# Optimization experiments

Measured on AMD Instinct MI355X. Metric: run time of the kernel, lower is better.

The kernel has to match this reference:

```python
import jax, jax.numpy as jnp
import numpy as np

N_PIX = 596   # (151-2)*(6-2) after two VALID 2x2 convs
HEADS, D = 4, 64

def _ln(x, axes, g=None, b=None, eps=1e-5):
    mu = jnp.mean(x, axes, keepdims=True)
    var = jnp.var(x, axes, keepdims=True)
    y = (x - mu) * jax.lax.rsqrt(var + eps)
    return y * g + b if g is not None else y

def _conv(x, w, b):
    y = jax.lax.conv_general_dilated(x, w, (1, 1), 'VALID',
                                     dimension_numbers=('NCHW', 'OIHW', 'NCHW'))
    return y + b[None, :, None, None]


def setup_inputs() -> dict:
    key = jax.random.key(0)
    ks = jax.random.split(key, 24)
    f32 = jnp.float32
    w = lambda k, s: jax.random.normal(k, s, f32) * 0.05
    inp = {
        'x': jax.random.normal(ks[0], (64, 4, 151, 6), f32),
        'conv1_w': w(ks[1], (16, 4, 2, 2)),  'conv1_b': w(ks[2], (16,)),
        'conv2_w': w(ks[3], (32, 16, 2, 2)), 'conv2_b': w(ks[4], (32,)),
        'kp_w': w(ks[5], (34, 256)),  'kp_b': w(ks[6], (256,)),
        'qp_w': w(ks[7], (34, 256)),  'qp_b': w(ks[8], (256,)),
        'vp_w': w(ks[9], (34, 256)),  'vp_b': w(ks[10], (256,)),
        'klin_w': w(ks[11], (64, N_PIX)), 'klin_b': w(ks[12], (N_PIX,)),
        'qlin_w': w(ks[13], (64, N_PIX)), 'qlin_b': w(ks[14], (N_PIX,)),
        'alin_w': w(ks[15], (N_PIX, N_PIX)), 'alin_b': w(ks[16], (N_PIX,)),
        'knorm_g': jnp.ones((HEADS, N_PIX, D), f32), 'knorm_b': jnp.zeros((HEADS, N_PIX, D), f32),
        'qnorm_g': jnp.ones((HEADS, N_PIX, D), f32), 'qnorm_b': jnp.zeros((HEADS, N_PIX, D), f32),
        'vnorm_g': jnp.ones((HEADS, N_PIX, D), f32), 'vnorm_b': jnp.zeros((HEADS, N_PIX, D), f32),
        'lin1_w': w(ks[17], (256, 64)), 'lin1_b': w(ks[18], (64,)),
        'lin2_w': w(ks[19], (64, 10)),  'lin2_b': w(ks[20], (10,)),
    }
    return inp


def reference(x, conv1_w, conv1_b, conv2_w, conv2_b,
              kp_w, kp_b, qp_w, qp_b, vp_w, vp_b,
              klin_w, klin_b, qlin_w, qlin_b, alin_w, alin_b,
              knorm_g, knorm_b, qnorm_g, qnorm_b, vnorm_g, vnorm_b,
              lin1_w, lin1_b, lin2_w, lin2_b):
    h = jax.nn.relu(_conv(x, conv1_w, conv1_b))
    h = jax.nn.relu(_conv(h, conv2_w, conv2_b))          # (N,32,149,4)
    N, C, cH, cW = h.shape
    xc = jnp.broadcast_to(jnp.arange(cW, dtype=h.dtype) / cW, (cH, cW))
    yc = jnp.broadcast_to((jnp.arange(cH, dtype=h.dtype) / cH)[:, None], (cH, cW))
    sp = jnp.broadcast_to(jnp.stack([xc, yc])[None], (N, 2, cH, cW))
    feats = jnp.concatenate([h, sp], axis=1).transpose(0, 2, 3, 1).reshape(N, N_PIX, C + 2)
    proj = lambda w_, b_: (feats @ w_ + b_).reshape(N, N_PIX, HEADS, D).transpose(0, 2, 1, 3)
    K = _ln(proj(kp_w, kp_b), (1, 2, 3), knorm_g, knorm_b)   # (N,h,596,64)
    Q = _ln(proj(qp_w, qp_b), (1, 2, 3), qnorm_g, qnorm_b)
    V = _ln(proj(vp_w, vp_b), (1, 2, 3), vnorm_g, vnorm_b)
    A = jax.nn.elu((Q @ qlin_w + qlin_b) + (K @ klin_w + klin_b))  # (N,h,596,596)
    A = jax.nn.softmax(A @ alin_w + alin_b, axis=-1)
    E = jnp.einsum('bhfc,bhcd->bhfd', A, V)                  # (N,h,596,64)
    E = E.transpose(0, 2, 1, 3).reshape(N, N_PIX, HEADS * D)
    E = jax.nn.relu(E @ lin1_w + lin1_b)
    E = _ln(E, (1, 2))                                       # LN over [596,64], no affine
    E = jnp.max(E, axis=1)                                   # (N,64)
    return jax.nn.elu(E @ lin2_w + lin2_b)                   # (N,10)
```

## Files before the change

kernel.cpp:

```cpp
#include <hip/hip_runtime.h>
#include <hip/hip_bf16.h>
#include <math.h>

typedef __hip_bfloat16 bf16;
typedef unsigned short ushort;
typedef __attribute__((ext_vector_type(8))) short short8;
typedef __attribute__((ext_vector_type(4))) float float4v;

#define BATCH 64
#define NPIX 596
#define CH 34
#define PC 256

static __device__ __forceinline__ ushort f2bu(float v){ bf16 h = __float2bfloat16(v); return *(ushort*)&h; }
static __device__ __forceinline__ float bu2f(ushort u){ bf16 h = *(bf16*)&u; return __bfloat162float(h); }
static __device__ __forceinline__ float eluf(float x){ return x > 0.f ? x : expm1f(x); }

__global__ __launch_bounds__(256) void k_conv_feats(
    const float* __restrict__ x,
    const float* __restrict__ w1, const float* __restrict__ b1,
    const float* __restrict__ w2, const float* __restrict__ b2,
    ushort* __restrict__ featsH, ushort* __restrict__ featsL)
{
  __shared__ float sw1[256];
  __shared__ float sb1[16];
  __shared__ float sw2[2048];
  __shared__ float sb2[32];
  __shared__ float h1[16*20*5];
  const int s = blockIdx.x, b = blockIdx.y, t = threadIdx.x;
  const float* xb = x + (size_t)b * 4*151*6;

  const int p0 = s*75;
  const int p1 = (p0+75 < NPIX) ? p0+75 : NPIX;
  const int rA = p0>>2, rB = (p1-1)>>2;
  const int nh = rB - rA + 2;

  sw1[t]=w1[t];
  if (t<16) sb1[t]=b1[t];
  for (int i=t;i<2048;i+=256) sw2[i]=w2[i];
  if (t<32) sb2[t]=b2[t];
  __syncthreads();

  for (int i=t; i<16*nh*5; i+=256){
    int oc = i/(nh*5), rem = i - oc*(nh*5);
    int lr = rem/5, cc = rem - (rem/5)*5;
    int r = rA + lr;
    float acc = sb1[oc];
    #pragma unroll
    for (int ic=0;ic<4;ic++){
      const float* xp = xb + ic*906 + r*6 + cc;
      const float* wp = sw1 + oc*16 + ic*4;
      acc += xp[0]*wp[0] + xp[1]*wp[1] + xp[6]*wp[2] + xp[7]*wp[3];
    }
    h1[(oc*20 + lr)*5 + cc] = fmaxf(acc, 0.f);
  }
  __syncthreads();

  const int np = p1 - p0;
  ushort* fbH = featsH + (size_t)b*NPIX*64;
  ushort* fbL = featsL + (size_t)b*NPIX*64;
  const short8 z8 = {0,0,0,0,0,0,0,0};
  for (int i=t;i<np*4;i+=256){
    int pl = i>>2, off = 32 + (i&3)*8;
    int p = p0 + pl;
    *(short8*)(fbH + (size_t)p*64 + off) = z8;
    *(short8*)(fbL + (size_t)p*64 + off) = z8;
  }
  for (int i=t;i<32*np;i+=256){
    int oc = i/np, pl = i - oc*np;
    int p = p0 + pl;
    int r = p>>2, cc = p&3;
    int lr = r - rA;
    float acc = sb2[oc];
    #pragma unroll
    for (int ic=0;ic<16;ic++){
      const float* hp = h1 + (ic*20 + lr)*5 + cc;
      const float* wp = sw2 + oc*64 + ic*4;
      acc += hp[0]*wp[0] + hp[1]*wp[1] + hp[5]*wp[2] + hp[6]*wp[3];
    }
    float v = fmaxf(acc, 0.f);
    ushort hu = f2bu(v);
    fbH[(size_t)p*64+oc] = hu;
    fbL[(size_t)p*64+oc] = f2bu(v - bu2f(hu));
  }
  __syncthreads();
  for (int pl=t; pl<np; pl+=256){
    int p = p0 + pl;
    float v1 = (float)(p&3)*0.25f;
    float v2 = (float)(p>>2)*(1.0f/149.0f);
    ushort h1u = f2bu(v1), h2u = f2bu(v2);
    fbH[(size_t)p*64+32] = h1u;  fbL[(size_t)p*64+32] = f2bu(v1 - bu2f(h1u));
    fbH[(size_t)p*64+33] = h2u;  fbL[(size_t)p*64+33] = f2bu(v2 - bu2f(h2u));
  }
}

__global__ __launch_bounds__(256) void k_prep(
    const float* __restrict__ aw, const float* __restrict__ qw, const float* __restrict__ kw,
    const float* __restrict__ l1w,
    const float* __restrict__ kpw, const float* __restrict__ qpw, const float* __restrict__ vpw,
    ushort* __restrict__ alinP, ushort* __restrict__ WqkP, ushort* __restrict__ w1T,
    ushort* __restrict__ projP)
{
  __shared__ float sA[4][32][17];
  const int t = threadIdx.x, w = t>>6, l = t&63;
  const int gw = blockIdx.x*4 + w;

  if (gw < 1016){
    const float* src; ushort* dst;
    int row0, col0, nrow, ncol, rstride; size_t slot;
    if (gw < 760){
      int tile = gw/19, kk = gw - tile*19;
      src = aw; rstride = NPIX; nrow = NPIX; ncol = NPIX;
      row0 = kk*32; col0 = tile*16;
      dst = alinP; slot = (size_t)gw*64;
    } else if (gw < 920){
      int g1 = gw - 760;
      int tile = g1>>2, kk = g1&3;
      rstride = NPIX; nrow = 64; ncol = NPIX;
      col0 = tile*16;
      if (kk < 2){ src = qw; row0 = kk*32; }
      else       { src = kw; row0 = (kk-2)*32; }
      dst = WqkP; slot = (size_t)g1*64;
    } else {
      int g2 = gw - 920;
      int which = g2>>5, rem = g2&31;
      int tile = rem>>1, kk = rem&1;
      src = which==0 ? kpw : which==1 ? qpw : vpw;
      rstride = PC; nrow = CH; ncol = PC;
      row0 = kk*32; col0 = tile*16;
      dst = projP; slot = (size_t)g2*64;
    }
    #pragma unroll
    for (int p=0;p<2;p++){
      int rr = p*16 + (l>>2);
      int r = row0 + rr;
      int cb = (l&3)*4;
      #pragma unroll
      for (int j=0;j<4;j++){
        int c = col0 + cb + j;
        float v = (r < nrow && c < ncol) ? src[(size_t)r*rstride + c] : 0.f;
        sA[w][rr][cb + j] = v;
      }
    }
    __syncthreads();
    int nloc = l&15, c0 = (l>>4)*8;
    ushort out[8];
    #pragma unroll
    for (int i=0;i<8;i++) out[i] = f2bu(sA[w][c0+i][nloc]);
    *(short8*)(dst + (slot + l)*8) = *(short8*)out;
  } else {
    int s3 = (gw - 1016)*64 + l;
    int n = s3>>5, e0 = (s3&31)*8;
    ushort out[8];
    #pragma unroll
    for (int i=0;i<8;i++) out[i] = f2bu(l1w[(size_t)(e0+i)*64 + n]);
    *(short8*)(w1T + (size_t)s3*8) = *(short8*)out;
  }
}

__global__ __launch_bounds__(256) void k_proj_p1(
    const ushort* __restrict__ featsH, const ushort* __restrict__ featsL,
    const ushort* __restrict__ projP,
    const float* __restrict__ kpb, const float* __restrict__ qpb, const float* __restrict__ vpb,
    float* __restrict__ statsP)
{
  __shared__ float red[8];
  const int rb = blockIdx.x, b = blockIdx.y, which = blockIdx.z;
  const int t = threadIdx.x, w = t>>6, l = t&63, quad = l>>4, ln = l&15;
  const float* Bv = which==0 ? kpb : which==1 ? qpb : vpb;

  float4v acc[4][4];
  #pragma unroll
  for (int ms=0;ms<4;ms++)
    #pragma unroll
    for (int i=0;i<4;i++) acc[ms][i] = (float4v){0.f,0.f,0.f,0.f};

  #pragma unroll
  for (int kk=0;kk<4;kk++){
    const ushort* fb = (kk<2 ? featsH : featsL) + (size_t)b*NPIX*64;
    short8 aq[4];
    #pragma unroll
    for (int ms=0;ms<4;ms++){
      int r = rb*64 + ms*16 + ln;
      short8 z = {0,0,0,0,0,0,0,0};
      aq[ms] = (r < NPIX) ? *(const short8*)(fb + (size_t)r*64 + (kk&1)*32 + quad*8) : z;
    }
    #pragma unroll
    for (int i=0;i<4;i++){
      int tile = w + 4*i;
      short8 bf = *(const short8*)(projP + ((size_t)((which*16 + tile)*2 + (kk&1))*64 + l)*8);
      #pragma unroll
      for (int ms=0;ms<4;ms++)
        acc[ms][i] = __builtin_amdgcn_mfma_f32_16x16x32_bf16(aq[ms], bf, acc[ms][i], 0,0,0);
    }
  }
  float s=0.f, s2=0.f;
  #pragma unroll
  for (int i=0;i<4;i++){
    int col = (w+4*i)*16 + ln;
    float bc = Bv[col];
    #pragma unroll
    for (int ms=0;ms<4;ms++)
      #pragma unroll
      for (int r=0;r<4;r++){
        int p = rb*64 + ms*16 + quad*4 + r;
        if (p < NPIX){
          float v = acc[ms][i][r] + bc;
          s += v; s2 += v*v;
        }
      }
  }
  #pragma unroll
  for (int o=32;o>0;o>>=1){ s += __shfl_down(s,o); s2 += __shfl_down(s2,o); }
  if (l==0){ red[w]=s; red[4+w]=s2; }
  __syncthreads();
  if (t==0){
    atomicAdd(&statsP[(which*64+b)*2],   red[0]+red[1]+red[2]+red[3]);
    atomicAdd(&statsP[(which*64+b)*2+1], red[4]+red[5]+red[6]+red[7]);
  }
}

__global__ __launch_bounds__(256) void k_proj_p2(
    const ushort* __restrict__ featsH, const ushort* __restrict__ featsL,
    const ushort* __restrict__ projP,
    const float* __restrict__ kpb, const float* __restrict__ qpb, const float* __restrict__ vpb,
    const float* __restrict__ kg, const float* __restrict__ kb_,
    const float* __restrict__ qg, const float* __restrict__ qb_,
    const float* __restrict__ vg, const float* __restrict__ vb_,
    const float* __restrict__ statsP,
    ushort* __restrict__ Kb, ushort* __restrict__ Qb, ushort* __restrict__ VP)
{
  __shared__ ushort vtile[64*264];
  const int rb = blockIdx.x, b = blockIdx.y, which = blockIdx.z;
  const int t = threadIdx.x, w = t>>6, l = t&63, quad = l>>4, ln = l&15;
  const float* Bv = which==0 ? kpb : which==1 ? qpb : vpb;
  const float* G  = which==0 ? kg  : which==1 ? qg  : vg;
  const float* Be = which==0 ? kb_ : which==1 ? qb_ : vb_;

  float4v acc[4][4];
  #pragma unroll
  for (int ms=0;ms<4;ms++)
    #pragma unroll
    for (int i=0;i<4;i++) acc[ms][i] = (float4v){0.f,0.f,0.f,0.f};

  #pragma unroll
  for (int kk=0;kk<4;kk++){
    const ushort* fb = (kk<2 ? featsH : featsL) + (size_t)b*NPIX*64;
    short8 aq[4];
    #pragma unroll
    for (int ms=0;ms<4;ms++){
      int r = rb*64 + ms*16 + ln;
      short8 z = {0,0,0,0,0,0,0,0};
      aq[ms] = (r < NPIX) ? *(const short8*)(fb + (size_t)r*64 + (kk&1)*32 + quad*8) : z;
    }
    #pragma unroll
    for (int i=0;i<4;i++){
      int tile = w + 4*i;
      short8 bf = *(const short8*)(projP + ((size_t)((which*16 + tile)*2 + (kk&1))*64 + l)*8);
      #pragma unroll
      for (int ms=0;ms<4;ms++)
        acc[ms][i] = __builtin_amdgcn_mfma_f32_16x16x32_bf16(aq[ms], bf, acc[ms][i], 0,0,0);
    }
  }
  const float n = (float)(NPIX*PC);
  const float S  = statsP[(which*64+b)*2];
  const float S2 = statsP[(which*64+b)*2+1];
  const float mu = S/n;
  const float rs = rsqrtf(S2/n - mu*mu + 1e-5f);

  if (which < 2){
    ushort* out = which==0 ? Kb : Qb;
    #pragma unroll
    for (int i=0;i<4;i++){
      int col = (w+4*i)*16 + ln;
      int h = col>>6, d = col&63;
      float bc = Bv[col];
      #pragma unroll
      for (int ms=0;ms<4;ms++)
        #pragma unroll
        for (int r=0;r<4;r++){
          int p = rb*64 + ms*16 + quad*4 + r;
          if (p < NPIX){
            int gi = (h*NPIX+p)*64 + d;
            float y = (acc[ms][i][r] + bc - mu)*rs*G[gi] + Be[gi];
            out[((size_t)(b*4+h)*NPIX + p)*64 + d] = f2bu(y);
          }
        }
    }
  } else {
    #pragma unroll
    for (int i=0;i<4;i++){
      int col = (w+4*i)*16 + ln;
      int h = col>>6, d = col&63;
      float bc = Bv[col];
      #pragma unroll
      for (int ms=0;ms<4;ms++)
        #pragma unroll
        for (int r=0;r<4;r++){
          int lrow = ms*16 + quad*4 + r;
          int p = rb*64 + lrow;
          ushort o = 0;
          if (p < NPIX){
            int gi = (h*NPIX+p)*64 + d;
            o = f2bu((acc[ms][i][r] + bc - mu)*rs*G[gi] + Be[gi]);
          }
          vtile[lrow*264 + col] = o;
        }
    }
    __syncthreads();
    #pragma unroll
    for (int e=0;e<8;e++){
      int sid = e*256 + t;
      int l2 = sid & 63;
      int rest = sid >> 6;
      int kkL = rest & 1, w2 = (rest>>1)&3, hh = rest>>3;
      int kk = rb*2 + kkL;
      if (kk < 19){
        int lrow0 = kkL*32 + ((l2>>4)<<3);
        int col = hh*64 + w2*16 + (l2&15);
        ushort o[8];
        #pragma unroll
        for (int jj=0;jj<8;jj++) o[jj] = vtile[(lrow0+jj)*264 + col];
        *(short8*)(VP + ((size_t)(b*4+hh)*4864 + (w2*19 + kk)*64 + l2)*8) = *(short8*)o;
      }
    }
  }
}

__global__ __launch_bounds__(256, 2) void k_attn(
    const ushort* __restrict__ Qb, const ushort* __restrict__ Kb,
    const ushort* __restrict__ alinP, const ushort* __restrict__ WqkP,
    const ushort* __restrict__ VP,
    const float* __restrict__ qbias, const float* __restrict__ kbias,
    const float* __restrict__ abias,
    ushort* __restrict__ Ew)
{
  extern __shared__ __align__(16) ushort sm[];
  ushort* strip = sm;
  float*  red   = (float*)(sm + 39424);

  const int t = threadIdx.x;
  const int w = t>>6, l = t&63, quad = l>>4, ln = l&15;
  const int id  = blockIdx.x + blockIdx.y*10;
  const int xcd = id & 7, idx = id >> 3;
  const int lin = xcd*320 + idx;
  const int bh  = lin/10, rb = lin - bh*10;
  const int b = bh>>2, h = bh&3;
  const int row0 = rb*64;
  const ushort* Qp = Qb + (size_t)bh*NPIX*64;
  const ushort* Kp = Kb + (size_t)bh*NPIX*64;

  float4v acc[4][10];
  #pragma unroll
  for (int ms=0;ms<4;ms++)
    #pragma unroll
    for (int i=0;i<10;i++) acc[ms][i] = (float4v){0.f,0.f,0.f,0.f};

  #pragma unroll
  for (int kk=0;kk<4;kk++){
    short8 aq[4];
    #pragma unroll
    for (int ms=0;ms<4;ms++){
      int r = row0 + ms*16 + ln;
      short8 z = {0,0,0,0,0,0,0,0};
      aq[ms] = (r < NPIX)
        ? *(const short8*)((kk<2 ? Qp : Kp) + (size_t)r*64 + (kk&1)*32 + quad*8) : z;
    }
    __builtin_amdgcn_s_setprio(1);
    #pragma unroll
    for (int i=0;i<10;i++){
      int tile = w + 4*i;
      short8 bf = *(const short8*)(WqkP + ((size_t)(tile*4 + kk)*64 + l)*8);
      #pragma unroll
      for (int ms=0;ms<4;ms++)
        acc[ms][i] = __builtin_amdgcn_mfma_f32_16x16x32_bf16(aq[ms], bf, acc[ms][i], 0,0,0);
    }
    __builtin_amdgcn_s_setprio(0);
  }
  #pragma unroll
  for (int i=0;i<10;i++){
    int t0 = w + 4*i;
    if (t0 < 38){
      int col = t0*16 + ln;
      bool cv = col < NPIX;
      float qkb = cv ? (qbias[col] + kbias[col]) : 0.f;
      #pragma unroll
      for (int ms=0;ms<4;ms++)
        #pragma unroll
        for (int r=0;r<4;r++){
          float v = 0.f;
          if (cv){ float xx = acc[ms][i][r] + qkb; v = xx > 0.f ? xx : __expf(xx) - 1.f; }
          strip[(ms*16+quad*4+r)*616 + col] = f2bu(v);
        }
    }
  }
  __syncthreads();

  #pragma unroll
  for (int ms=0;ms<4;ms++)
    #pragma unroll
    for (int i=0;i<10;i++) acc[ms][i] = (float4v){0.f,0.f,0.f,0.f};
  #pragma unroll 4
  for (int kk=0;kk<19;kk++){
    short8 af[4];
    #pragma unroll
    for (int ms=0;ms<4;ms++)
      af[ms] = *(const short8*)(strip + (ms*16+ln)*616 + kk*32 + quad*8);
    __builtin_amdgcn_s_setprio(1);
    #pragma unroll
    for (int i=0;i<10;i++){
      int tile = w + 4*i;
      short8 bf = *(const short8*)(alinP + ((size_t)(tile*19 + kk)*64 + l)*8);
      #pragma unroll
      for (int ms=0;ms<4;ms++)
        acc[ms][i] = __builtin_amdgcn_mfma_f32_16x16x32_bf16(af[ms], bf, acc[ms][i], 0,0,0);
    }
    __builtin_amdgcn_s_setprio(0);
  }
  __syncthreads();

  float sum[4][4];
  #pragma unroll
  for (int ms=0;ms<4;ms++)
    #pragma unroll
    for (int r=0;r<4;r++) sum[ms][r] = 0.f;
  #pragma unroll
  for (int i=0;i<10;i++){
    int t0 = w + 4*i;
    if (t0 < 38){
      int col = t0*16 + ln;
      bool cv = col < NPIX;
      float ab = cv ? abias[col] : 0.f;
      #pragma unroll
      for (int ms=0;ms<4;ms++)
        #pragma unroll
        for (int r=0;r<4;r++){
          float e = cv ? __expf(acc[ms][i][r] + ab) : 0.f;
          sum[ms][r] += e;
          strip[(ms*16+quad*4+r)*616 + col] = f2bu(e);
        }
    }
  }
  #pragma unroll
  for (int ms=0;ms<4;ms++)
    #pragma unroll
    for (int r=0;r<4;r++)
      #pragma unroll
      for (int o=8;o>0;o>>=1) sum[ms][r] += __shfl_xor(sum[ms][r], o, 16);
  if (ln==0){
    #pragma unroll
    for (int ms=0;ms<4;ms++)
      #pragma unroll
      for (int r=0;r<4;r++) red[(ms*16+quad*4+r)*4 + w] = sum[ms][r];
  }
  __syncthreads();

  float4v ve[4];
  #pragma unroll
  for (int ms=0;ms<4;ms++) ve[ms] = (float4v){0.f,0.f,0.f,0.f};
  #pragma unroll
  for (int kk=0;kk<19;kk++){
    short8 bf = *(const short8*)(VP + ((size_t)bh*4864 + (w*19 + kk)*64 + l)*8);
    __builtin_amdgcn_s_setprio(1);
    #pragma unroll
    for (int ms=0;ms<4;ms++){
      short8 af = *(const short8*)(strip + (ms*16+ln)*616 + kk*32 + quad*8);
      ve[ms] = __builtin_amdgcn_mfma_f32_16x16x32_bf16(af, bf, ve[ms], 0,0,0);
    }
    __builtin_amdgcn_s_setprio(0);
  }
  #pragma unroll
  for (int ms=0;ms<4;ms++)
    #pragma unroll
    for (int r=0;r<4;r++){
      int p = row0 + ms*16 + quad*4 + r;
      if (p < NPIX){
        float4v v = *(float4v*)&red[(ms*16+quad*4+r)*4];
        float inv = 1.f / (v[0]+v[1]+v[2]+v[3]);
        Ew[((size_t)b*NPIX + p)*256 + h*64 + w*16 + ln] = f2bu(ve[ms][r] * inv);
      }
    }
}

__global__ __launch_bounds__(256) void k_lin1(
    const ushort* __restrict__ Ew, const ushort* __restrict__ w1T,
    const float* __restrict__ bias,
    float* __restrict__ F, float* __restrict__ stats)
{
  __shared__ ushort sw1[64*264];
  __shared__ float red[8];
  const int t = threadIdx.x;
  const int w = t>>6, l = t&63, quad = l>>4, ln = l&15;
  const int rb = blockIdx.x, b = blockIdx.y;
  for (int g=t; g<2048; g+=256){
    int row = g>>5, q = g&31;
    *(short8*)(sw1 + row*264 + q*8) = *(const short8*)(w1T + row*256 + q*8);
  }
  __syncthreads();
  float4v acc[4];
  #pragma unroll
  for (int ms=0;ms<4;ms++) acc[ms] = (float4v){0.f,0.f,0.f,0.f};
  #pragma unroll
  for (int kk=0;kk<8;kk++){
    short8 bf = *(const short8*)(sw1 + (w*16+ln)*264 + kk*32 + quad*8);
    #pragma unroll
    for (int ms=0;ms<4;ms++){
      int p = rb*64 + ms*16 + ln;
      size_t rowi = (size_t)b*NPIX + (p < NPIX ? p : 0);
      short8 a = *(const short8*)(Ew + rowi*256 + kk*32 + quad*8);
      acc[ms] = __builtin_amdgcn_mfma_f32_16x16x32_bf16(a, bf, acc[ms], 0,0,0);
    }
  }
  const int col = w*16 + ln;
  const float bc = bias[col];
  float s=0.f, s2=0.f;
  #pragma unroll
  for (int ms=0;ms<4;ms++)
    #pragma unroll
    for (int r=0;r<4;r++){
      int p = rb*64 + ms*16 + quad*4 + r;
      if (p < NPIX){
        float v = fmaxf(acc[ms][r] + bc, 0.f);
        F[((size_t)b*NPIX + p)*64 + col] = v;
        s += v; s2 += v*v;
      }
    }
  #pragma unroll
  for (int o=32;o>0;o>>=1){ s += __shfl_down(s,o); s2 += __shfl_down(s2,o); }
  if (l==0){ red[w]=s; red[4+w]=s2; }
  __syncthreads();
  if (t==0){
    atomicAdd(&stats[b*2],   red[0]+red[1]+red[2]+red[3]);
    atomicAdd(&stats[b*2+1], red[4]+red[5]+red[6]+red[7]);
  }
}

__global__ __launch_bounds__(256) void k_final(
    const float* __restrict__ F, const float* __restrict__ stats,
    const float* __restrict__ w2, const float* __restrict__ b2v,
    float* __restrict__ out)
{
  __shared__ float cm[256];
  __shared__ float nm[64];
  const int b = blockIdx.x, t = threadIdx.x;
  const int d = t&63, grp = t>>6;
  const float* Fb = F + (size_t)b*NPIX*64;
  float m = -1e30f;
  for (int p=grp;p<NPIX;p+=4) m = fmaxf(m, Fb[p*64+d]);
  cm[t]=m;
  __syncthreads();
  if (t<64){
    float mm = fmaxf(fmaxf(cm[t],cm[t+64]), fmaxf(cm[t+128],cm[t+192]));
    const float n = (float)(NPIX*64);
    float S = stats[b*2], S2 = stats[b*2+1];
    float mu = S/n, var = S2/n - mu*mu;
    nm[t] = (mm - mu) * rsqrtf(var + 1e-5f);
  }
  __syncthreads();
  if (t<10){
    float acc = b2v[t];
    for (int e=0;e<64;e++) acc += nm[e]*w2[e*10+t];
    out[b*10+t] = eluf(acc);
  }
}

extern "C" void kernel_launch(void* const* d_in, const int* in_sizes, int n_in,
                              void* d_out, int out_size, void* d_ws, size_t ws_size,
                              hipStream_t stream)
{
  const float* x       = (const float*)d_in[0];
  const float* conv1_w = (const float*)d_in[1];
  const float* conv1_b = (const float*)d_in[2];
  const float* conv2_w = (const float*)d_in[3];
  const float* conv2_b = (const float*)d_in[4];
  const float* kp_w    = (const float*)d_in[5];
  const float* kp_b    = (const float*)d_in[6];
  const float* qp_w    = (const float*)d_in[7];
  const float* qp_b    = (const float*)d_in[8];
  const float* vp_w    = (const float*)d_in[9];
  const float* vp_b    = (const float*)d_in[10];
  const float* klin_w  = (const float*)d_in[11];
  const float* klin_b  = (const float*)d_in[12];
  const float* qlin_w  = (const float*)d_in[13];
  const float* qlin_b  = (const float*)d_in[14];
  const float* alin_w  = (const float*)d_in[15];
  const float* alin_b  = (const float*)d_in[16];
  const float* knorm_g = (const float*)d_in[17];
  const float* knorm_b = (const float*)d_in[18];
  const float* qnorm_g = (const float*)d_in[19];
  const float* qnorm_b = (const float*)d_in[20];
  const float* vnorm_g = (const float*)d_in[21];
  const float* vnorm_b = (const float*)d_in[22];
  const float* lin1_w  = (const float*)d_in[23];
  const float* lin1_b  = (const float*)d_in[24];
  const float* lin2_w  = (const float*)d_in[25];
  const float* lin2_b  = (const float*)d_in[26];

  float* feats  = (float*)d_ws;
  float* F      = feats + (size_t)BATCH*NPIX*CH;
  float* statsE = F + (size_t)BATCH*NPIX*64;
  float* statsP = statsE + 128;
  ushort* Qb    = (ushort*)(statsP + 384);
  ushort* Kb    = Qb + (size_t)BATCH*4*NPIX*64;
  ushort* Vb    = Kb + (size_t)BATCH*4*NPIX*64;
  ushort* Ew    = Vb + (size_t)BATCH*4*NPIX*64;
  ushort* w1T   = Ew + (size_t)BATCH*NPIX*256;
  ushort* alinP = w1T + 16384;
  ushort* WqkP  = alinP + 389120;
  ushort* VP    = WqkP + 81920;
  ushort* projP = VP + 9961472;
  ushort* featsH = (ushort*)feats;
  ushort* featsL = (ushort*)F;

  hipMemsetAsync(statsE, 0, 512*sizeof(float), stream);

  dim3 gc(8, BATCH);
  k_conv_feats<<<gc, 256, 0, stream>>>(x, conv1_w, conv1_b, conv2_w, conv2_b, featsH, featsL);

  k_prep<<<262, 256, 0, stream>>>(alin_w, qlin_w, klin_w, lin1_w, kp_w, qp_w, vp_w,
                                  alinP, WqkP, w1T, projP);

  dim3 gp(10, BATCH, 3);
  k_proj_p1<<<gp, 256, 0, stream>>>(featsH, featsL, projP, kp_b, qp_b, vp_b, statsP);
  k_proj_p2<<<gp, 256, 0, stream>>>(featsH, featsL, projP, kp_b, qp_b, vp_b,
                                    knorm_g, knorm_b, qnorm_g, qnorm_b, vnorm_g, vnorm_b,
                                    statsP, Kb, Qb, VP);

  static bool attr_set = false;
  if (!attr_set){
    hipFuncSetAttribute((const void*)k_attn, hipFuncAttributeMaxDynamicSharedMemorySize, 79872);
    attr_set = true;
  }

  dim3 ga(10, BATCH*4);
  k_attn<<<ga, 256, 79872, stream>>>(Qb, Kb, alinP, WqkP, VP,
                                     qlin_b, klin_b, alin_b, Ew);

  dim3 gl(10, BATCH);
  k_lin1<<<gl, 256, 0, stream>>>(Ew, w1T, lin1_b, F, statsE);

  k_final<<<BATCH, 256, 0, stream>>>(F, statsE, lin2_w, lin2_b, (float*)d_out);
}
```

Before: 601.9 us.

## Split attention block across eight waves and divide PV reduction across halves

```diff
diff --git a/kernel.cpp b/kernel.cpp
--- a/kernel.cpp
+++ b/kernel.cpp
@@ -327,7 +327,7 @@
   }
 }
 
-__global__ __launch_bounds__(256, 2) void k_attn(
+__global__ __launch_bounds__(512, 4) void k_attn(
     const ushort* __restrict__ Qb, const ushort* __restrict__ Kb,
     const ushort* __restrict__ alinP, const ushort* __restrict__ WqkP,
     const ushort* __restrict__ VP,
@@ -338,6 +338,7 @@
   extern __shared__ __align__(16) ushort sm[];
   ushort* strip = sm;
   float*  red   = (float*)(sm + 39424);
+  float*  rsum  = (float*)(sm + 40448);
 
   const int t = threadIdx.x;
   const int w = t>>6, l = t&63, quad = l>>4, ln = l&15;
@@ -350,11 +351,11 @@
   const ushort* Qp = Qb + (size_t)bh*NPIX*64;
   const ushort* Kp = Kb + (size_t)bh*NPIX*64;
 
-  float4v acc[4][10];
+  float4v acc[4][5];
   #pragma unroll
   for (int ms=0;ms<4;ms++)
     #pragma unroll
-    for (int i=0;i<10;i++) acc[ms][i] = (float4v){0.f,0.f,0.f,0.f};
+    for (int i=0;i<5;i++) acc[ms][i] = (float4v){0.f,0.f,0.f,0.f};
 
   #pragma unroll
   for (int kk=0;kk<4;kk++){
@@ -368,8 +369,8 @@
     }
     __builtin_amdgcn_s_setprio(1);
     #pragma unroll
-    for (int i=0;i<10;i++){
-      int tile = w + 4*i;
+    for (int i=0;i<5;i++){
+      int tile = w + 8*i;
       short8 bf = *(const short8*)(WqkP + ((size_t)(tile*4 + kk)*64 + l)*8);
       #pragma unroll
       for (int ms=0;ms<4;ms++)
@@ -378,8 +379,8 @@
     __builtin_amdgcn_s_setprio(0);
   }
   #pragma unroll
-  for (int i=0;i<10;i++){
-    int t0 = w + 4*i;
+  for (int i=0;i<5;i++){
+    int t0 = w + 8*i;
     if (t0 < 38){
       int col = t0*16 + ln;
       bool cv = col < NPIX;
@@ -399,8 +400,7 @@
   #pragma unroll
   for (int ms=0;ms<4;ms++)
     #pragma unroll
-    for (int i=0;i<10;i++) acc[ms][i] = (float4v){0.f,0.f,0.f,0.f};
-  #pragma unroll 4
+    for (int i=0;i<5;i++) acc[ms][i] = (float4v){0.f,0.f,0.f,0.f};
   for (int kk=0;kk<19;kk++){
     short8 af[4];
     #pragma unroll
@@ -408,8 +408,8 @@
       af[ms] = *(const short8*)(strip + (ms*16+ln)*616 + kk*32 + quad*8);
     __builtin_amdgcn_s_setprio(1);
     #pragma unroll
-    for (int i=0;i<10;i++){
-      int tile = w + 4*i;
+    for (int i=0;i<5;i++){
+      int tile = w + 8*i;
       short8 bf = *(const short8*)(alinP + ((size_t)(tile*19 + kk)*64 + l)*8);
       #pragma unroll
       for (int ms=0;ms<4;ms++)
@@ -425,8 +425,8 @@
     #pragma unroll
     for (int r=0;r<4;r++) sum[ms][r] = 0.f;
   #pragma unroll
-  for (int i=0;i<10;i++){
-    int t0 = w + 4*i;
+  for (int i=0;i<5;i++){
+    int t0 = w + 8*i;
     if (t0 < 38){
       int col = t0*16 + ln;
       bool cv = col < NPIX;
@@ -451,35 +451,57 @@
     #pragma unroll
     for (int ms=0;ms<4;ms++)
       #pragma unroll
-      for (int r=0;r<4;r++) red[(ms*16+quad*4+r)*4 + w] = sum[ms][r];
-  }
-  __syncthreads();
-
+      for (int r=0;r<4;r++) red[(ms*16+quad*4+r)*8 + w] = sum[ms][r];
+  }
+  __syncthreads();
+  if (t < 64){
+    float4v v0 = *(float4v*)&red[t*8];
+    float4v v1 = *(float4v*)&red[t*8+4];
+    rsum[t] = (v0[0]+v0[1]+v0[2]+v0[3]) + (v1[0]+v1[1]+v1[2]+v1[3]);
+  }
+  __syncthreads();
+
+  const int half = w>>2, wc = w&3;
   float4v ve[4];
   #pragma unroll
   for (int ms=0;ms<4;ms++) ve[ms] = (float4v){0.f,0.f,0.f,0.f};
-  #pragma unroll
-  for (int kk=0;kk<19;kk++){
-    short8 bf = *(const short8*)(VP + ((size_t)bh*4864 + (w*19 + kk)*64 + l)*8);
-    __builtin_amdgcn_s_setprio(1);
-    #pragma unroll
-    for (int ms=0;ms<4;ms++){
-      short8 af = *(const short8*)(strip + (ms*16+ln)*616 + kk*32 + quad*8);
-      ve[ms] = __builtin_amdgcn_mfma_f32_16x16x32_bf16(af, bf, ve[ms], 0,0,0);
-    }
-    __builtin_amdgcn_s_setprio(0);
-  }
-  #pragma unroll
-  for (int ms=0;ms<4;ms++)
-    #pragma unroll
-    for (int r=0;r<4;r++){
-      int p = row0 + ms*16 + quad*4 + r;
-      if (p < NPIX){
-        float4v v = *(float4v*)&red[(ms*16+quad*4+r)*4];
-        float inv = 1.f / (v[0]+v[1]+v[2]+v[3]);
-        Ew[((size_t)b*NPIX + p)*256 + h*64 + w*16 + ln] = f2bu(ve[ms][r] * inv);
+  {
+    const int kkA = half ? 10 : 0;
+    const int kkB = half ? 19 : 10;
+    for (int kk=kkA; kk<kkB; kk++){
+      short8 bf = *(const short8*)(VP + ((size_t)bh*4864 + (wc*19 + kk)*64 + l)*8);
+      __builtin_amdgcn_s_setprio(1);
+      #pragma unroll
+      for (int ms=0;ms<4;ms++){
+        short8 af = *(const short8*)(strip + (ms*16+ln)*616 + kk*32 + quad*8);
+        ve[ms] = __builtin_amdgcn_mfma_f32_16x16x32_bf16(af, bf, ve[ms], 0,0,0);
       }
-    }
+      __builtin_amdgcn_s_setprio(0);
+    }
+  }
+  __syncthreads();
+  float* scr = (float*)sm;
+  if (half){
+    #pragma unroll
+    for (int ms=0;ms<4;ms++)
+      #pragma unroll
+      for (int r=0;r<4;r++)
+        scr[(ms*16+quad*4+r)*64 + wc*16 + ln] = ve[ms][r];
+  }
+  __syncthreads();
+  if (!half){
+    #pragma unroll
+    for (int ms=0;ms<4;ms++)
+      #pragma unroll
+      for (int r=0;r<4;r++){
+        int lrow = ms*16 + quad*4 + r;
+        int p = row0 + lrow;
+        if (p < NPIX){
+          float v = ve[ms][r] + scr[lrow*64 + wc*16 + ln];
+          Ew[((size_t)b*NPIX + p)*256 + h*64 + wc*16 + ln] = f2bu(v / rsum[lrow]);
+        }
+      }
+  }
 }
 
 __global__ __launch_bounds__(256) void k_lin1(
@@ -628,12 +650,12 @@
 
   static bool attr_set = false;
   if (!attr_set){
-    hipFuncSetAttribute((const void*)k_attn, hipFuncAttributeMaxDynamicSharedMemorySize, 79872);
+    hipFuncSetAttribute((const void*)k_attn, hipFuncAttributeMaxDynamicSharedMemorySize, 81152);
     attr_set = true;
   }
 
   dim3 ga(10, BATCH*4);
-  k_attn<<<ga, 256, 79872, stream>>>(Qb, Kb, alinP, WqkP, VP,
+  k_attn<<<ga, 512, 81152, stream>>>(Qb, Kb, alinP, WqkP, VP,
                                      qlin_b, klin_b, alin_b, Ew);
 
   dim3 gl(10, BATCH);
```

Result: faster. 560.4 us (-6.9%).
